# Kernel optimization log

Hardware: AMD Instinct MI355X
Metric: run time of the kernel (lower is better)

## Reference

```python
import jax, jax.numpy as jnp
import numpy as np

FS = 32000
HOP = 512
WIN_SIZES = [2048, 1024, 512, 256, 128, 64]
BAND_EDGES = [20.0, 80.0, 500.0, 1250.0, 2540.0, 4050.0, 15000.0]
ERB_STEP = 0.25
ERBS = np.arange(1.75, 39.0 + 1e-6, ERB_STEP)            # 150 ERB channels
FC = (10.0 ** (ERBS / 21.366) - 1.0) / 0.004368           # channel center freqs (Hz)
I0 = (2e-5) ** 2                                          # reference intensity (Pa^2)
LUT_X = np.linspace(0.0, 110.0, 88).astype(np.float32)    # LUT excitation grid (dB)
SIGMA = 0.08
P_INHIB = 1.5978
HALF = 8
_g = np.arange(-HALF, HALF + 1) * ERB_STEP
GAUSS = np.exp(-_g ** 2 / (2.0 * SIGMA ** 2))
GAUSS = (GAUSS / GAUSS.sum()).astype(np.float32)

def _components():
    # frequency-dependent window selection: longest window -> lowest band
    freqs, idxs = [], []
    for w, N in enumerate(WIN_SIZES):
        fb = np.arange(N // 2 + 1) * FS / N
        sel = np.where((fb >= BAND_EDGES[w]) & (fb < BAND_EDGES[w + 1]))[0]
        idxs.append(sel)
        freqs.append(fb[sel])
    return np.concatenate(freqs), idxs
COMP_FREQS, WIN_BIN_IDX = _components()  # K ~ 67 sparse components

def _roex():
    erbw = 24.673 * (0.004368 * FC + 1.0)
    p = 4.0 * FC / erbw
    g = np.abs(COMP_FREQS[:, None] / FC[None, :] - 1.0)
    return ((1.0 + p * g) * np.exp(-p * g)).astype(np.float32)
ROEX_W = _roex()  # (K, 150)

def _ear_filter(x, h):
    # Stage 1: outer/middle ear FIR, same-length output
    B, C, T = x.shape
    k = h[::-1].reshape(1, 1, -1)
    y = jax.lax.conv_general_dilated(x.reshape(B * C, 1, T), k, (1,),
                                     [(h.shape[0] // 2, h.shape[0] // 2)],
                                     dimension_numbers=("NCH", "OIH", "NCH"))
    return y.reshape(B, C, T)

def _sparse_spectrum(x):
    # Stage 2: multi-resolution FFT analysis -> linear intensities at sparse comps
    B, T = x.shape
    F = T // HOP
    pad = WIN_SIZES[0] // 2
    xp = jnp.pad(x, ((0, 0), (pad, pad)))
    centers = pad + jnp.arange(F) * HOP
    outs = []
    for N, bins in zip(WIN_SIZES, WIN_BIN_IDX):
        idx = (centers - N // 2)[:, None] + jnp.arange(N)   # (F, N)
        frames = xp[:, idx]                                 # (B, F, N)
        n = jnp.arange(N, dtype=x.dtype)
        win = 0.5 - 0.5 * jnp.cos(2.0 * jnp.pi * n / (N - 1))
        spec = jnp.fft.rfft(frames * win, axis=-1)
        amp = 2.0 * jnp.abs(spec[..., jnp.asarray(bins)]) / win.sum()
        outs.append(0.5 * amp ** 2)                          # tone intensity
    return jnp.concatenate(outs, axis=-1)                    # (B, F, K)

def _agc(x, a_att, a_rel):
    # asymmetric attack/release AGC over frame axis (axis=1)
    def step(s, xt):
        a = jnp.where(xt > s, a_att, a_rel)
        s = a * xt + (1.0 - a) * s
        return s, s
    xt = jnp.moveaxis(x, 1, 0)
    _, y = jax.lax.scan(step, jnp.zeros_like(xt[0]), xt)
    return jnp.moveaxis(y, 0, 1)

def _smooth(n):
    # Gaussian spatial smoothing along ERB-channel axis
    B, F, C = n.shape
    k = jnp.asarray(GAUSS[::-1].copy(), n.dtype).reshape(1, 1, -1)
    y = jax.lax.conv_general_dilated(n.reshape(B * F, 1, C), k, (1,),
                                     [(HALF, HALF)],
                                     dimension_numbers=("NCH", "OIH", "NCH"))
    return y.reshape(B, F, C)

def _forward(audio, ear_fir, lut_values):
    y = _ear_filter(audio, ear_fir)
    lut_x = jnp.asarray(LUT_X)
    W = jnp.asarray(ROEX_W, audio.dtype)
    stl = []
    for ch in range(2):
        I = _sparse_spectrum(y[:, ch])                       # (B, F, K)
        E = I @ W                                            # roex excitation (B, F, 150)
        E_db = 10.0 * jnp.log10(E / I0 + 1e-12)
        n_inst = jnp.interp(jnp.clip(E_db, lut_x[0], lut_x[-1]), lut_x, lut_values)
        stl.append(_agc(n_inst, 0.045, 0.033))               # short-term loudness
    sl, sr = _smooth(stl[0]), _smooth(stl[1])
    sech = lambda z: 1.0 / jnp.cosh(z)
    stl_l = (sl * sech(P_INHIB * sr)).sum(-1) / 4.0          # (B, F)
    stl_r = (sr * sech(P_INHIB * sl)).sum(-1) / 4.0
    ltl_l = _agc(stl_l[..., None], 0.01, 0.00133)[..., 0]
    ltl_r = _agc(stl_r[..., None], 0.01, 0.00133)[..., 0]
    sLoud = stl_l + stl_r
    lLoud = ltl_l + ltl_r
    mLoud = lLoud.max(axis=-1)
    return sLoud, lLoud, mLoud

def setup_inputs():
    key = jax.random.key(0)
    k1, k2, k3 = jax.random.split(key, 3)
    audio = jax.random.normal(k1, (16, 2, 320000), dtype=jnp.float32) * 0.05
    ear_fir = jax.random.normal(k2, (1025,), dtype=jnp.float32) * 0.03
    lut_values = jnp.sort(jax.random.uniform(k3, (88,), dtype=jnp.float32)) * 40.0
    return {"audio": audio, "ear_fir": ear_fir, "lut_values": lut_values}

def reference(audio, ear_fir, lut_values):
    return _forward(audio, ear_fir, lut_values)
```

## Files before the change

kernel.cpp:

```cpp
#include <hip/hip_runtime.h>
#include <hip/hip_bf16.h>
#include <math.h>

#define T_LEN   320000
#define NB      16
#define NROWS   32
#define NFRAMES 625
#define NCOMP   67
#define NCH     150
#define HOPSZ   512

typedef __attribute__((ext_vector_type(8))) _Float16 half8v;
typedef __attribute__((ext_vector_type(8))) short short8v;
typedef __attribute__((ext_vector_type(4))) float f32x4;

__constant__ int cW_N[6]  = {2048,1024,512,256,128,64};
__constant__ int cW_K0[6] = {2,3,8,10,11,9};
__constant__ int cW_CB[7] = {0,4,17,29,40,46,67};
__constant__ int cW_CO[7] = {0,8192,21504,27648,30464,31232,32576};
__constant__ int dNEp[6]  = {3072,2048,1536,1280,1152,1152};
__constant__ int dNEr[6]  = {3072,2048,1536,1280,1152,1088};
__constant__ int dBTb[7]  = {0,147456,245760,319488,380928,436224,491520};
__constant__ int dCPB[6]  = {12,8,6,5,5,5};
__constant__ int dCKB[7]  = {0,48,152,224,279,309,414};
__constant__ int eW[8] = {0,0,0,1,2,3,4,5};
__constant__ int eF[8] = {0,1,624,0,0,0,0,0};

__constant__ int tBb[12]   = {147456,180224,0,380928,0,436224,245760,454656,270336,473088,319488,339968};
__constant__ int tNEp[12]  = {2048,2048,3072,1152,3072,1152,1536,1152,1536,1152,1280,1280};
__constant__ int tStb[12]  = {512,512,0,960,0,992,768,992,768,992,896,896};
__constant__ int tKs0[12]  = {0,0,0,0,48,0,0,0,0,0,0,0};
__constant__ int tKs1[12]  = {64,64,48,36,96,36,48,36,48,36,40,40};
__constant__ int tJadd[12] = {4,12,0,40,0,46,17,54,25,62,29,37};
__constant__ int tNbL[12]  = {13,5,4,6,4,21,12,13,4,5,11,3};
__constant__ int tMode[12] = {0,0,1,0,2,0,0,0,0,0,0,0};
__constant__ int wStart[8] = {0,1,2,4,6,8,10,11};
__constant__ int wCnt[8]   = {1,1,2,2,2,2,1,1};

__device__ __forceinline__ unsigned short f2bf(float v) {
  unsigned u = __float_as_uint(v);
  return (unsigned short)((u + 0x7FFFu + ((u >> 16) & 1u)) >> 16);
}

__global__ __launch_bounds__(256) void setup_k(const float* __restrict__ h,
                                               const float* __restrict__ x,
                                               float2* __restrict__ coeff,
                                               float* __restrict__ Wmat,
                                               float* __restrict__ gauss,
                                               unsigned short* __restrict__ Bf,
                                               float* __restrict__ ye,
                                               unsigned short* __restrict__ Wb16) {
  __shared__ float sm[3585];
  const int bid = blockIdx.x, tid = threadIdx.x;
  if (bid < 167) {
    int gid = bid * 256 + tid;
    if (gid < 32576) {
      int w = 0;
      while (gid >= cW_CO[w + 1]) ++w;
      int local = gid - cW_CO[w];
      int N = cW_N[w];
      int jloc = local / N;
      int n = local - jloc * N;
      int k = cW_K0[w] + jloc;
      float win = 0.5f - 0.5f * cospif(2.0f * (float)n / (float)(N - 1));
      int r = (int)(((long long)k * (long long)n) % (long long)N);
      float ang = 2.0f * (float)r / (float)N;
      float scale = sqrtf(2.0f) / (0.5f * (float)(N - 1));
      float wc = win * scale;
      coeff[gid] = make_float2(wc * cospif(ang), wc * sinpif(ang));
    } else if (gid < 32576 + NCOMP * NCH) {
      int t = gid - 32576;
      int j = t / NCH, c = t - j * NCH;
      float erb = 1.75f + 0.25f * (float)c;
      float fc = (exp10f(erb * (1.0f / 21.366f)) - 1.0f) * (1.0f / 0.004368f);
      float erbw = 24.673f * (0.004368f * fc + 1.0f);
      float p = 4.0f * fc / erbw;
      int w = 0;
      while (j >= cW_CB[w + 1]) ++w;
      float freq = (float)(cW_K0[w] + (j - cW_CB[w])) * (32000.0f / (float)cW_N[w]);
      float g = fabsf(freq / fc - 1.0f);
      float pg = p * g;
      Wmat[j * NCH + c] = (1.0f + pg) * expf(-pg);
    } else if (gid == 32576 + NCOMP * NCH) {
      float tmp[17]; float s = 0.0f;
      for (int k = 0; k < 17; ++k) {
        float g = ((float)k - 8.0f) * 0.25f;
        tmp[k] = expf(-g * g / (2.0f * 0.08f * 0.08f));
        s += tmp[k];
      }
      for (int k = 0; k < 17; ++k) gauss[k] = tmp[k] / s;
    }
  } else if (bid < 581) {
    float* cre_l = sm;
    float* cim_l = sm + 1280;
    float* hs    = sm + 2560;
    const int b2 = bid - 167;
    int w = 0;
    while (b2 >= dCKB[w + 1]) ++w;
    const int local = b2 - dCKB[w];
    const int jloc = local / dCPB[w];
    const int chunk = local - jloc * dCPB[w];
    const int N = cW_N[w];
    const int k = cW_K0[w] + jloc;
    const int NEp = dNEp[w], NEr = dNEr[w];
    const int v0 = chunk * 256;
    const int nlo_blk = max(0, v0 - 1024);
    const int nhi_blk = min(N - 1, v0 + 255);
    const int cnt_n = nhi_blk - nlo_blk + 1;
    const float scale = sqrtf(2.0f) / (0.5f * (float)(N - 1));
    for (int i = tid; i < 1025; i += 256) hs[i] = h[i];
    for (int i = tid; i < cnt_n; i += 256) {
      int n = nlo_blk + i;
      float win = 0.5f - 0.5f * cospif(2.0f * (float)n / (float)(N - 1));
      int r = (int)(((long long)k * (long long)n) % (long long)N);
      float ang = 2.0f * (float)r / (float)N;
      float wc = win * scale;
      cre_l[i] = wc * cospif(ang);
      cim_l[i] = wc * sinpif(ang);
    }
    __syncthreads();
    const int v = v0 + tid;
    if (v >= NEp) return;
    float re = 0.0f, im = 0.0f;
    if (v < NEr) {
      const int n0 = max(nlo_blk, v - 1024);
      const int n1 = min(nhi_blk, v);
      for (int n = n0; n <= n1; ++n) {
        float hv = hs[n + 1024 - v];
        re = fmaf(cre_l[n - nlo_blk], hv, re);
        im = fmaf(cim_l[n - nlo_blk], hv, im);
      }
    }
    size_t o0 = (size_t)dBTb[w] + (size_t)(2 * jloc) * NEp + v;
    size_t o1 = o0 + NEp;
    _Float16 hr = (_Float16)re;
    _Float16 hi2 = (_Float16)im;
    Bf[o0] = *(unsigned short*)&hr;
    Bf[o1] = *(unsigned short*)&hi2;
  } else if (bid < 965) {
    float* xl = sm;
    float* hs = sm + 1280;
    const int b2 = bid - 581;
    const int chunk = b2 % 12, row = b2 / 12;
    const size_t rowoff = (size_t)row * T_LEN;
    const int i0 = chunk * 256;
    const int pos0 = (i0 < 1536) ? i0 : 318464 + (i0 - 1536);
    for (int i = tid; i < 1025; i += 256) hs[i] = h[i];
    for (int i = tid; i < 1280; i += 256) {
      int g = pos0 - 512 + i;
      xl[i] = ((unsigned)g < (unsigned)T_LEN) ? x[rowoff + g] : 0.0f;
    }
    __syncthreads();
    float a0 = 0.0f, a1 = 0.0f, a2 = 0.0f, a3 = 0.0f;
    const int d = tid + 1024;
    for (int m = 0; m < 1024; m += 4) {
      a0 = fmaf(hs[m],     xl[d - m],     a0);
      a1 = fmaf(hs[m + 1], xl[d - m - 1], a1);
      a2 = fmaf(hs[m + 2], xl[d - m - 2], a2);
      a3 = fmaf(hs[m + 3], xl[d - m - 3], a3);
    }
    float acc = ((a0 + a1) + (a2 + a3)) + hs[1024] * xl[d - 1024];
    ye[(size_t)row * 3072 + i0 + tid] = acc;
  } else {
    for (int u = tid; u < 160 * 96; u += 256) {
      int c = u / 96, j = u - (u / 96) * 96;
      float val = 0.0f;
      if (c < NCH && j < NCOMP) {
        float erb = 1.75f + 0.25f * (float)c;
        float fc = (exp10f(erb * (1.0f / 21.366f)) - 1.0f) * (1.0f / 0.004368f);
        float erbw = 24.673f * (0.004368f * fc + 1.0f);
        float p = 4.0f * fc / erbw;
        int w = 0;
        while (j >= cW_CB[w + 1]) ++w;
        float freq = (float)(cW_K0[w] + (j - cW_CB[w])) * (32000.0f / (float)cW_N[w]);
        float g = fabsf(freq / fc - 1.0f);
        float pg = p * g;
        val = (1.0f + pg) * expf(-pg);
      }
      Wb16[u] = f2bf(val);
    }
  }
}

#define TILE_X 18944
#define SWZ4(i) ((i) ^ ((((i) >> 9) & 15) << 3))

__global__ __launch_bounds__(512) void sparse2(const float* __restrict__ x,
                                               const unsigned short* __restrict__ Bf,
                                               const float2* __restrict__ coeff,
                                               const float* __restrict__ ye,
                                               float* __restrict__ Ibuf) {
  __shared__ __align__(16) unsigned short sxh[TILE_X];
  __shared__ float redA[512];
  const int b = blockIdx.x, tid = threadIdx.x;
  if (b < 640) {
    const int fblk = b % 20, row = b / 20;
    const int f0 = fblk * 32;
    const float* xr = x + (size_t)row * T_LEN;
    const int lo = f0 * HOPSZ - 1536;
    for (int i = 4 * tid; i < TILE_X; i += 2048) {
      const int g = lo + i;
      float v[4];
      if (g >= 0 && g + 4 <= T_LEN) {
        float4 p = *(const float4*)(xr + g);
        v[0] = p.x; v[1] = p.y; v[2] = p.z; v[3] = p.w;
      } else {
#pragma unroll
        for (int q = 0; q < 4; ++q) {
          int gg = g + q;
          v[q] = ((unsigned)gg < (unsigned)T_LEN) ? xr[gg] : 0.0f;
        }
      }
      unsigned short h4[4];
#pragma unroll
      for (int q = 0; q < 4; ++q) {
        _Float16 hv = (_Float16)v[q];
        h4[q] = *(unsigned short*)&hv;
      }
      const int is = SWZ4(i);
      *(ushort4*)(sxh + is) = make_ushort4(h4[0], h4[1], h4[2], h4[3]);
    }
    __syncthreads();
    const int wv = tid >> 6, lane = tid & 63;
    const int fidx = lane & 15, kg = lane >> 4;
    const int t0 = wStart[wv], tcnt = wCnt[wv];
    f32x4 pA = (f32x4){0.f,0.f,0.f,0.f};
    f32x4 pB = (f32x4){0.f,0.f,0.f,0.f};
    for (int ti = t0; ti < t0 + tcnt; ++ti) {
      const int NEp = tNEp[ti];
      const int ks0 = tKs0[ti], ks1 = tKs1[ti];
      const unsigned short* Bp = Bf + tBb[ti] + fidx * NEp + kg * 8;
      const int ibase = fidx * 512 + tStb[ti] + kg * 8;
      f32x4 acc0 = (f32x4){0.f,0.f,0.f,0.f};
      f32x4 acc1 = (f32x4){0.f,0.f,0.f,0.f};
#pragma unroll 2
      for (int kk = ks0; kk < ks1; ++kk) {
        const int ko = kk * 32;
        half8v bv = *(const half8v*)(Bp + ko);
        half8v a0 = *(const half8v*)(sxh + SWZ4(ibase + ko));
        half8v a1 = *(const half8v*)(sxh + SWZ4(ibase + 8192 + ko));
        acc0 = __builtin_amdgcn_mfma_f32_16x16x32_f16(a0, bv, acc0, 0, 0, 0);
        acc1 = __builtin_amdgcn_mfma_f32_16x16x32_f16(a1, bv, acc1, 0, 0, 0);
      }
      const int mode = tMode[ti];
      if (mode == 0) {
        const int jadd = tJadd[ti], nbl = tNbL[ti];
        const int fh = fidx >> 1;
        const bool jvalid = !(fidx & 1) && fh < nbl;
#pragma unroll
        for (int r = 0; r < 4; ++r) {
          float v0 = acc0[r];
          float sq0 = v0 * v0;
          sq0 += __shfl_xor(sq0, 1);
          int fA = f0 + kg * 4 + r;
          if (jvalid && fA != 0)
            Ibuf[((size_t)row * NFRAMES + fA) * NCOMP + jadd + fh] = sq0;
          float v1 = acc1[r];
          float sq1 = v1 * v1;
          sq1 += __shfl_xor(sq1, 1);
          int fB = f0 + 16 + kg * 4 + r;
          if (jvalid && fB < NFRAMES)
            Ibuf[((size_t)row * NFRAMES + fB) * NCOMP + jadd + fh] = sq1;
        }
      } else if (mode == 1) {
#pragma unroll
        for (int r = 0; r < 4; ++r) {
          redA[lane * 4 + r] = acc0[r];
          redA[256 + lane * 4 + r] = acc1[r];
        }
      } else {
        pA = acc0; pB = acc1;
      }
    }
    __syncthreads();
    if (wv == 3) {
#pragma unroll
      for (int r = 0; r < 4; ++r) {
        float v0 = pA[r] + redA[lane * 4 + r];
        float sq0 = v0 * v0;
        sq0 += __shfl_xor(sq0, 1);
        int fA = f0 + kg * 4 + r;
        float v1 = pB[r] + redA[256 + lane * 4 + r];
        float sq1 = v1 * v1;
        sq1 += __shfl_xor(sq1, 1);
        int fB = f0 + 16 + kg * 4 + r;
        if (!(fidx & 1)) {
          int j = fidx >> 1;
          if (j < 4) {
            bool eA = (fA == 0) || (fA == 1) || (fA == 624);
            if (!eA) Ibuf[((size_t)row * NFRAMES + fA) * NCOMP + j] = sq0;
            bool eB = (fB == 1) || (fB == 624);
            if (fB < NFRAMES && !eB) Ibuf[((size_t)row * NFRAMES + fB) * NCOMP + j] = sq1;
          }
        }
      }
    }
  } else {
    const int row = b - 640;
    float* yl = (float*)sxh;
    for (int i = tid; i < 3072; i += 512) yl[i] = ye[(size_t)row * 3072 + i];
    __syncthreads();
    const int wv = tid >> 6, lane = tid & 63;
    const int w = eW[wv], f = eF[wv];
    const int N = cW_N[w];
    const int nb = cW_CB[w + 1] - cW_CB[w];
    for (int jl = 0; jl < nb; ++jl) {
      const float2* cf = coeff + cW_CO[w] + (size_t)jl * N;
      float re = 0.0f, im = 0.0f;
      for (int n = lane; n < N; n += 64) {
        int pos = f * HOPSZ - (N >> 1) + n;
        if ((unsigned)pos < (unsigned)T_LEN) {
          int yi = (pos < 1536) ? pos : (pos - 318464 + 1536);
          float yv = yl[yi];
          float2 cs = cf[n];
          re = fmaf(yv, cs.x, re);
          im = fmaf(yv, cs.y, im);
        }
      }
#pragma unroll
      for (int off = 32; off > 0; off >>= 1) {
        re += __shfl_xor(re, off);
        im += __shfl_xor(im, off);
      }
      if (lane == 0)
        Ibuf[((size_t)row * NFRAMES + f) * NCOMP + (cW_CB[w] + jl)] = re * re + im * im;
    }
  }
}

__global__ __launch_bounds__(256) void espec(const float* __restrict__ Ibuf,
                                             const unsigned short* __restrict__ Wb16,
                                             const float* __restrict__ lut,
                                             float* __restrict__ ninst) {
  __shared__ __align__(16) unsigned short sxA[64 * 104];
  __shared__ float luts[88];
  const int row = blockIdx.y;
  const int fB = blockIdx.x * 64;
  const int tid = threadIdx.x;
  if (tid < 88) luts[tid] = lut[tid];
  for (int u = tid; u < 64 * 52; u += 256) ((unsigned*)sxA)[u] = 0;
  __syncthreads();
  for (int u = tid; u < 64 * NCOMP; u += 256) {
    int fl = u / NCOMP, j = u - fl * NCOMP;
    int f = fB + fl;
    float v = (f < NFRAMES) ? Ibuf[((size_t)row * NFRAMES + f) * NCOMP + j] : 0.0f;
    sxA[fl * 104 + j] = f2bf(v);
  }
  __syncthreads();
  const int wv = tid >> 6, lane = tid & 63;
  const int fidx = lane & 15, kg = lane >> 4;
  const unsigned short* Ap = sxA + (wv * 16 + fidx) * 104 + kg * 8;
  short8v a0 = *(const short8v*)(Ap);
  short8v a1 = *(const short8v*)(Ap + 32);
  short8v a2 = *(const short8v*)(Ap + 64);
  f32x4 acc[10];
#pragma unroll
  for (int ct = 0; ct < 10; ++ct) acc[ct] = (f32x4){0.f,0.f,0.f,0.f};
#pragma unroll
  for (int ct = 0; ct < 10; ++ct) {
    const unsigned short* Bp = Wb16 + (ct * 16 + fidx) * 96 + kg * 8;
    short8v b0 = *(const short8v*)(Bp);
    short8v b1 = *(const short8v*)(Bp + 32);
    short8v b2 = *(const short8v*)(Bp + 64);
    acc[ct] = __builtin_amdgcn_mfma_f32_16x16x32_bf16(a0, b0, acc[ct], 0, 0, 0);
    acc[ct] = __builtin_amdgcn_mfma_f32_16x16x32_bf16(a1, b1, acc[ct], 0, 0, 0);
    acc[ct] = __builtin_amdgcn_mfma_f32_16x16x32_bf16(a2, b2, acc[ct], 0, 0, 0);
  }
  const int fbase = fB + wv * 16 + kg * 4;
#pragma unroll
  for (int ct = 0; ct < 10; ++ct) {
    const int c = ct * 16 + fidx;
    if (c < NCH) {
#pragma unroll
      for (int r = 0; r < 4; ++r) {
        const int f = fbase + r;
        if (f < NFRAMES) {
          float e = acc[ct][r];
          float edb = 3.0102999566f * __log2f(fmaf(e, 2.5e9f, 1e-12f));
          float xv = fminf(fmaxf(edb, 0.0f), 110.0f);
          float u2 = xv * (87.0f / 110.0f);
          int i0 = (int)u2; if (i0 > 86) i0 = 86;
          float fr = u2 - (float)i0;
          ninst[((size_t)row * NFRAMES + f) * NCH + c] =
              fmaf(luts[i0 + 1] - luts[i0], fr, luts[i0]);
        }
      }
    }
  }
}

__global__ __launch_bounds__(64) void agc1(const float* __restrict__ ninst,
                                           float* __restrict__ stl) {
  int idx = blockIdx.x * 64 + threadIdx.x;
  if (idx >= NROWS * NCH) return;
  int row = idx / NCH, c = idx - row * NCH;
  const float* src = ninst + (size_t)row * NFRAMES * NCH + c;
  float* dst = stl + (size_t)row * NFRAMES * NCH + c;
  float buf[16], cur[16];
#pragma unroll
  for (int i = 0; i < 16; ++i) buf[i] = src[(size_t)i * NCH];
  float s = 0.0f;
  for (int fb = 0; fb < 608; fb += 16) {
#pragma unroll
    for (int i = 0; i < 16; ++i) cur[i] = buf[i];
#pragma unroll
    for (int i = 0; i < 16; ++i) buf[i] = src[(size_t)(fb + 16 + i) * NCH];
#pragma unroll
    for (int j = 0; j < 16; ++j) {
      float xv = cur[j];
      float a = (xv > s) ? 0.045f : 0.033f;
      s = a * xv + (1.0f - a) * s;
      dst[(size_t)(fb + j) * NCH] = s;
    }
  }
#pragma unroll
  for (int j = 0; j < 16; ++j) {
    float xv = buf[j];
    float a = (xv > s) ? 0.045f : 0.033f;
    s = a * xv + (1.0f - a) * s;
    dst[(size_t)(608 + j) * NCH] = s;
  }
  float xv = src[(size_t)624 * NCH];
  float a = (xv > s) ? 0.045f : 0.033f;
  s = a * xv + (1.0f - a) * s;
  dst[(size_t)624 * NCH] = s;
}

__global__ __launch_bounds__(256) void combine(const float* __restrict__ stl,
                                               const float* __restrict__ gauss,
                                               float* __restrict__ outL,
                                               float* __restrict__ outR) {
  __shared__ float sl[8][168], sr[8][168], gsh[17];
  const int b = blockIdx.y, fb = blockIdx.x * 8;
  const int tid = threadIdx.x;
  if (tid < 17) gsh[tid] = gauss[tid];
  for (int u = tid; u < 8 * 168; u += 256) {
    int fi = u / 168, c = u - fi * 168;
    sl[fi][c] = 0.0f; sr[fi][c] = 0.0f;
  }
  __syncthreads();
  for (int u = tid; u < 8 * 300; u += 256) {
    int fi = u / 300, r = u - fi * 300;
    int f = fb + fi;
    if (f < NFRAMES) {
      int ch = (r < NCH) ? 0 : 1;
      int c = (r < NCH) ? r : r - NCH;
      float v = stl[((size_t)(b * 2 + ch) * NFRAMES + f) * NCH + c];
      if (ch == 0) sl[fi][8 + c] = v; else sr[fi][8 + c] = v;
    }
  }
  __syncthreads();
  const int wv = tid >> 6, lane = tid & 63;
#pragma unroll
  for (int fi2 = 0; fi2 < 2; ++fi2) {
    const int fi = wv * 2 + fi2;
    const int f = fb + fi;
    float pvl = 0.0f, pvr = 0.0f;
#pragma unroll
    for (int s = 0; s < 3; ++s) {
      int c = lane + 64 * s;
      if (c < NCH) {
        float smL = 0.0f, smR = 0.0f;
#pragma unroll
        for (int t = 0; t < 17; ++t) {
          smL = fmaf(gsh[t], sl[fi][c + t], smL);
          smR = fmaf(gsh[t], sr[fi][c + t], smR);
        }
        float tR = __expf(-1.5978f * smR);
        float tL = __expf(-1.5978f * smL);
        pvl += smL * (2.0f * tR / fmaf(tR, tR, 1.0f));
        pvr += smR * (2.0f * tL / fmaf(tL, tL, 1.0f));
      }
    }
#pragma unroll
    for (int off = 32; off > 0; off >>= 1) {
      pvl += __shfl_xor(pvl, off);
      pvr += __shfl_xor(pvr, off);
    }
    if (lane == 0 && f < NFRAMES) {
      outL[b * NFRAMES + f] = pvl * 0.25f;
      outR[b * NFRAMES + f] = pvr * 0.25f;
    }
  }
}

__global__ __launch_bounds__(256) void final_k(const float* __restrict__ sLst,
                                               const float* __restrict__ sRst,
                                               float* __restrict__ out) {
  __shared__ float Ls[NB][641];
  __shared__ float Rs[NB][641];
  __shared__ float Lv[NB][641];
  const int tid = threadIdx.x;
  for (int u = tid; u < NB * NFRAMES; u += 256) {
    int b = u / NFRAMES, f = u - b * NFRAMES;
    float a = sLst[u];
    float c = sRst[u];
    Ls[b][f] = a;
    Rs[b][f] = c;
    out[u] = a + c;
  }
  __syncthreads();
  if (tid < NB) {
    const int b = tid;
    float ll = 0.0f, lr = 0.0f, mx = -3.4e38f;
    for (int f = 0; f < NFRAMES; ++f) {
      float a = Ls[b][f];
      float c = Rs[b][f];
      float aa = (a > ll) ? 0.01f : 0.00133f;
      ll = aa * a + (1.0f - aa) * ll;
      float ab = (c > lr) ? 0.01f : 0.00133f;
      lr = ab * c + (1.0f - ab) * lr;
      float lv = ll + lr;
      Lv[b][f] = lv;
      mx = fmaxf(mx, lv);
    }
    out[2 * NB * NFRAMES + b] = mx;
  }
  __syncthreads();
  for (int u = tid; u < NB * NFRAMES; u += 256) {
    int b = u / NFRAMES, f = u - b * NFRAMES;
    out[NB * NFRAMES + u] = Lv[b][f];
  }
}

extern "C" void kernel_launch(void* const* d_in, const int* in_sizes, int n_in,
                              void* d_out, int out_size, void* d_ws, size_t ws_size,
                              hipStream_t stream) {
  const float* audio = (const float*)d_in[0];
  const float* ear   = (const float*)d_in[1];
  const float* lut   = (const float*)d_in[2];
  char* ws = (char*)d_ws;

  unsigned short* BfT    = (unsigned short*)(ws);
  float2*         coeffO = (float2*)(ws + 983040);
  float*          Wmat   = (float*)(ws + 1243648);
  float*          gauss  = (float*)(ws + 1283848);
  float*          yedge  = (float*)(ws + 1284176);
  float*          Ibuf   = (float*)(ws + 1677392);
  float*          ninst  = (float*)(ws + 7037392);
  float*          stl    = (float*)(ws + 19037392);
  float*          stlL   = (float*)(ws + 31037392);
  float*          stlR   = (float*)(ws + 31077392);
  unsigned short* Wb16   = (unsigned short*)(ws + 31117392);

  hipLaunchKernelGGL(setup_k, dim3(966), dim3(256), 0, stream,
                     ear, audio, coeffO, Wmat, gauss, BfT, yedge, Wb16);
  hipLaunchKernelGGL(sparse2, dim3(672), dim3(512), 0, stream,
                     audio, BfT, coeffO, yedge, Ibuf);
  hipLaunchKernelGGL(espec, dim3(10, 32), dim3(256), 0, stream, Ibuf, Wb16, lut, ninst);
  hipLaunchKernelGGL(agc1, dim3(75), dim3(64), 0, stream, ninst, stl);
  hipLaunchKernelGGL(combine, dim3(79, 16), dim3(256), 0, stream, stl, gauss, stlL, stlR);
  hipLaunchKernelGGL(final_k, dim3(1), dim3(256), 0, stream, stlL, stlR, (float*)d_out);
}
```

Baseline: 196.6 us.

## Replicate fused FIR-DFT basis into 8 copies and unroll basis-building dot product

The setup kernel now writes the fp16 fused ear-filter/DFT basis matrix into eight separate copies in the workspace, and each sparse2 block reads the copy selected by its block index. This spreads the heavily shared basis reads across more memory addresses, likely aiming at L2/channel contention or cache-slice hotspotting on the multi-die MI355X. The basis-building inner loop is also unrolled by four with independent accumulators to shorten the FMA dependency chain. In exchange, setup does eight times the basis stores, the workspace grows, and every later buffer offset shifts.

```diff
diff --git a/kernel.cpp b/kernel.cpp
--- a/kernel.cpp
+++ b/kernel.cpp
@@ -9,6 +9,8 @@
 #define NCOMP   67
 #define NCH     150
 #define HOPSZ   512
+#define BREP    8
+#define BSZ     491520
 
 typedef __attribute__((ext_vector_type(8))) _Float16 half8v;
 typedef __attribute__((ext_vector_type(8))) short short8v;
@@ -125,18 +127,37 @@
     if (v < NEr) {
       const int n0 = max(nlo_blk, v - 1024);
       const int n1 = min(nhi_blk, v);
-      for (int n = n0; n <= n1; ++n) {
-        float hv = hs[n + 1024 - v];
-        re = fmaf(cre_l[n - nlo_blk], hv, re);
-        im = fmaf(cim_l[n - nlo_blk], hv, im);
-      }
+      float r0 = 0.f, r1 = 0.f, r2 = 0.f, r3 = 0.f;
+      float m0 = 0.f, m1 = 0.f, m2 = 0.f, m3 = 0.f;
+      int n = n0;
+      const int hoff = 1024 - v, coff = -nlo_blk;
+      for (; n + 3 <= n1; n += 4) {
+        float h0 = hs[n + hoff],     h1 = hs[n + 1 + hoff];
+        float h2 = hs[n + 2 + hoff], h3 = hs[n + 3 + hoff];
+        r0 = fmaf(cre_l[n + coff],     h0, r0); m0 = fmaf(cim_l[n + coff],     h0, m0);
+        r1 = fmaf(cre_l[n + 1 + coff], h1, r1); m1 = fmaf(cim_l[n + 1 + coff], h1, m1);
+        r2 = fmaf(cre_l[n + 2 + coff], h2, r2); m2 = fmaf(cim_l[n + 2 + coff], h2, m2);
+        r3 = fmaf(cre_l[n + 3 + coff], h3, r3); m3 = fmaf(cim_l[n + 3 + coff], h3, m3);
+      }
+      for (; n <= n1; ++n) {
+        float hv = hs[n + hoff];
+        r0 = fmaf(cre_l[n + coff], hv, r0);
+        m0 = fmaf(cim_l[n + coff], hv, m0);
+      }
+      re = (r0 + r1) + (r2 + r3);
+      im = (m0 + m1) + (m2 + m3);
     }
     size_t o0 = (size_t)dBTb[w] + (size_t)(2 * jloc) * NEp + v;
     size_t o1 = o0 + NEp;
     _Float16 hr = (_Float16)re;
     _Float16 hi2 = (_Float16)im;
-    Bf[o0] = *(unsigned short*)&hr;
-    Bf[o1] = *(unsigned short*)&hi2;
+    unsigned short hrb = *(unsigned short*)&hr;
+    unsigned short hib = *(unsigned short*)&hi2;
+#pragma unroll
+    for (int cp = 0; cp < BREP; ++cp) {
+      Bf[(size_t)cp * BSZ + o0] = hrb;
+      Bf[(size_t)cp * BSZ + o1] = hib;
+    }
   } else if (bid < 965) {
     float* xl = sm;
     float* hs = sm + 1280;
@@ -197,6 +218,7 @@
     const int fblk = b % 20, row = b / 20;
     const int f0 = fblk * 32;
     const float* xr = x + (size_t)row * T_LEN;
+    const unsigned short* Bc = Bf + (size_t)(b & (BREP - 1)) * BSZ;
     const int lo = f0 * HOPSZ - 1536;
     for (int i = 4 * tid; i < TILE_X; i += 2048) {
       const int g = lo + i;
@@ -229,7 +251,7 @@
     for (int ti = t0; ti < t0 + tcnt; ++ti) {
       const int NEp = tNEp[ti];
       const int ks0 = tKs0[ti], ks1 = tKs1[ti];
-      const unsigned short* Bp = Bf + tBb[ti] + fidx * NEp + kg * 8;
+      const unsigned short* Bp = Bc + tBb[ti] + fidx * NEp + kg * 8;
       const int ibase = fidx * 512 + tStb[ti] + kg * 8;
       f32x4 acc0 = (f32x4){0.f,0.f,0.f,0.f};
       f32x4 acc1 = (f32x4){0.f,0.f,0.f,0.f};
@@ -532,16 +554,16 @@
   char* ws = (char*)d_ws;
 
   unsigned short* BfT    = (unsigned short*)(ws);
-  float2*         coeffO = (float2*)(ws + 983040);
-  float*          Wmat   = (float*)(ws + 1243648);
-  float*          gauss  = (float*)(ws + 1283848);
-  float*          yedge  = (float*)(ws + 1284176);
-  float*          Ibuf   = (float*)(ws + 1677392);
-  float*          ninst  = (float*)(ws + 7037392);
-  float*          stl    = (float*)(ws + 19037392);
-  float*          stlL   = (float*)(ws + 31037392);
-  float*          stlR   = (float*)(ws + 31077392);
-  unsigned short* Wb16   = (unsigned short*)(ws + 31117392);
+  float2*         coeffO = (float2*)(ws + 7864320);
+  float*          Wmat   = (float*)(ws + 8124928);
+  float*          gauss  = (float*)(ws + 8165128);
+  float*          yedge  = (float*)(ws + 8165376);
+  float*          Ibuf   = (float*)(ws + 8558592);
+  float*          ninst  = (float*)(ws + 13918592);
+  float*          stl    = (float*)(ws + 25918592);
+  float*          stlL   = (float*)(ws + 37918592);
+  float*          stlR   = (float*)(ws + 37958592);
+  unsigned short* Wb16   = (unsigned short*)(ws + 37998592);
 
   hipLaunchKernelGGL(setup_k, dim3(966), dim3(256), 0, stream,
                      ear, audio, coeffO, Wmat, gauss, BfT, yedge, Wb16);
```

New measurement: 184.4 us. 1.07x faster.
